# Performance work log

Measured on AMD Instinct MI355X. Metric: run time of the kernel, lower is better.

Reference implementation:

```python
import jax, jax.numpy as jnp
import numpy as np

DEPTH = 7  # complete binary trees with 2**DEPTH = 128 leaves

B, L = 4096, 128
V, E, OUT = 100000, 128, 3


def setup_inputs() -> dict:
    key = jax.random.key(0)
    ks = jax.random.split(key, 6)
    tokens = jax.random.randint(ks[0], (B, L), 0, V, dtype=jnp.int64)
    embedding = jax.random.normal(ks[1], (V, E), dtype=jnp.float32)
    # tree_layer: Linear(2E -> E); torch stores weight as [out, in]
    W_tree = jax.random.normal(ks[2], (E, 2 * E), dtype=jnp.float32) * (1.0 / np.sqrt(2 * E))
    b_tree = jax.random.normal(ks[3], (E,), dtype=jnp.float32) * 0.01
    # classifier_layer: Linear(E -> OUT)
    W_cls = jax.random.normal(ks[4], (OUT, E), dtype=jnp.float32) * (1.0 / np.sqrt(E))
    b_cls = jax.random.normal(ks[5], (OUT,), dtype=jnp.float32) * 0.01
    return {"tokens": tokens, "embedding": embedding, "W_tree": W_tree,
            "b_tree": b_tree, "W_cls": W_cls, "b_cls": b_cls}


def reference(tokens, embedding, W_tree, b_tree, W_cls, b_cls):
    # Leaf embeddings: gather rows of the embedding table. [B, L, E]
    reps = embedding[tokens]
    # Level-synchronous bottom-up composition (depth-batched across all trees):
    # at each level, pair adjacent nodes, concat features, apply tree_layer + tanh.
    for _ in range(DEPTH):
        left = reps[:, 0::2, :]   # [B, n/2, E]
        right = reps[:, 1::2, :]  # [B, n/2, E]
        combined = jnp.concatenate([left, right], axis=-1)  # [B, n/2, 2E]
        reps = jnp.tanh(jnp.einsum('bnh,eh->bne', combined, W_tree) + b_tree)
    roots = reps[:, 0, :]  # [B, E]
    return roots @ W_cls.T + b_cls  # [B, OUT]
```

## Files before the change

### kernel.cpp

```cpp
#include <hip/hip_runtime.h>
#include <hip/hip_fp16.h>


typedef _Float16 half8 __attribute__((ext_vector_type(8)));
typedef float floatx4 __attribute__((ext_vector_type(4)));

#define STRIDE 264
#define UROW   33
#define NPAIR  2048

__device__ __forceinline__ float fast_tanh(float x) {
  float e = __expf(2.f * x);
  return 1.f - 2.f * __builtin_amdgcn_rcpf(e + 1.f);
}

__device__ __forceinline__ unsigned pkrtz(float a, float b) {
  auto h = __builtin_amdgcn_cvt_pkrtz(a, b);
  return __builtin_bit_cast(unsigned, h);
}

__device__ __forceinline__ void gather_leafhalf(int tok, const float* __restrict__ emb,
                                                _Float16* buf, int row, int seg) {
  const float4* src = (const float4*)emb + (size_t)tok * 32 + (seg & 1) * 16;
  uint4* dst = (uint4*)buf + row * UROW + seg * 8;
#pragma unroll
  for (int j = 0; j < 8; ++j) {
    float4 x = src[2 * j], y = src[2 * j + 1];
    uint4 w;
    w.x = pkrtz(x.x, x.y); w.y = pkrtz(x.z, x.w);
    w.z = pkrtz(y.x, y.y); w.w = pkrtz(y.z, y.w);
    dst[j] = w;
  }
}

__device__ __forceinline__ void mfma_k256(const _Float16* arow, const half8 (&Wf)[2][8],
                                          floatx4 (&accO)[2]) {
  floatx4 aA[2], aB[2];
  aA[0] = (floatx4){0.f, 0.f, 0.f, 0.f}; aA[1] = (floatx4){0.f, 0.f, 0.f, 0.f};
  aB[0] = (floatx4){0.f, 0.f, 0.f, 0.f}; aB[1] = (floatx4){0.f, 0.f, 0.f, 0.f};
#pragma unroll
  for (int ks = 0; ks < 4; ++ks) {
    half8 x0 = *(const half8*)(arow + ks * 32);
    half8 x1 = *(const half8*)(arow + (ks + 4) * 32);
    aA[0] = __builtin_amdgcn_mfma_f32_16x16x32_f16(x0, Wf[0][ks],     aA[0], 0, 0, 0);
    aB[0] = __builtin_amdgcn_mfma_f32_16x16x32_f16(x1, Wf[0][ks + 4], aB[0], 0, 0, 0);
    aA[1] = __builtin_amdgcn_mfma_f32_16x16x32_f16(x0, Wf[1][ks],     aA[1], 0, 0, 0);
    aB[1] = __builtin_amdgcn_mfma_f32_16x16x32_f16(x1, Wf[1][ks + 4], aB[1], 0, 0, 0);
  }
  accO[0] = aA[0] + aB[0];
  accO[1] = aA[1] + aB[1];
}

template<int MT, int MOUT>
__device__ __forceinline__ void level_std(
    const _Float16* inb, _Float16* outb,
    const half8 (&Wf)[2][8], const float (&bias)[2],
    int nbase, int l15, int quad)
{
  floatx4 acc[MT][2];
  if (MT == 1) {
    floatx4 a2[2];
    mfma_k256(inb + l15 * STRIDE + quad * 8, Wf, a2);
    acc[0][0] = a2[0]; acc[0][1] = a2[1];
  } else {
#pragma unroll
    for (int m = 0; m < MT; ++m) {
      acc[m][0] = (floatx4){0.f, 0.f, 0.f, 0.f};
      acc[m][1] = (floatx4){0.f, 0.f, 0.f, 0.f};
    }
#pragma unroll
    for (int m = 0; m < MT; ++m) {
      const _Float16* arow = inb + (m * 16 + l15) * STRIDE + quad * 8;
#pragma unroll
      for (int ks = 0; ks < 8; ++ks) {
        half8 a = *(const half8*)(arow + ks * 32);
        acc[m][0] = __builtin_amdgcn_mfma_f32_16x16x32_f16(a, Wf[0][ks], acc[m][0], 0, 0, 0);
        acc[m][1] = __builtin_amdgcn_mfma_f32_16x16x32_f16(a, Wf[1][ks], acc[m][1], 0, 0, 0);
      }
    }
  }

  const int mrow = quad * 4;
#pragma unroll
  for (int m = 0; m < MT; ++m)
#pragma unroll
    for (int i = 0; i < 2; ++i) {
      const int col = (nbase + i) * 16 + l15;
#pragma unroll
      for (int r = 0; r < 4; ++r) {
        const int node = m * 16 + mrow + r;
        if (node < MOUT) {
          float v = fast_tanh(acc[m][i][r] + bias[i]);
          outb[(node >> 1) * STRIDE + (node & 1) * 128 + col] = (_Float16)v;
        }
      }
    }
}

__global__ __launch_bounds__(256, 3)
void tree_kernel(const int* __restrict__ tokens,
                 const float* __restrict__ embedding,
                 const float* __restrict__ W_tree,
                 const float* __restrict__ b_tree,
                 const float* __restrict__ W_cls,
                 const float* __restrict__ b_cls,
                 float* __restrict__ out)
{
  __shared__ __align__(16) _Float16 bufA[64 * STRIDE];
  __shared__ __align__(16) _Float16 bufB[32 * STRIDE];
  __shared__ __align__(16) _Float16 bufC[4 * STRIDE];
  __shared__ float wavepart[4][2][3];

  const int tid  = threadIdx.x;
  const int wid  = tid >> 6;
  const int lane = tid & 63;
  const int l15  = lane & 15;
  const int quad = lane >> 4;
  const int nbase = wid * 2;
  const int row  = tid & 63;
  const int seg  = tid >> 6;
  const int tidx = 2 * row + (seg >> 1);

  half8 Wf[2][8];
#pragma unroll
  for (int i = 0; i < 2; ++i) {
    const int e = (nbase + i) * 16 + l15;
#pragma unroll
    for (int ks = 0; ks < 8; ++ks) {
      const int k = ks * 32 + quad * 8;
      const float4* p = (const float4*)(W_tree + e * 256 + k);
      float4 lo = p[0], hi = p[1];
      half8 f;
      f[0] = (_Float16)lo.x; f[1] = (_Float16)lo.y; f[2] = (_Float16)lo.z; f[3] = (_Float16)lo.w;
      f[4] = (_Float16)hi.x; f[5] = (_Float16)hi.y; f[6] = (_Float16)hi.z; f[7] = (_Float16)hi.w;
      Wf[i][ks] = f;
    }
  }
  float bias[2];
#pragma unroll
  for (int i = 0; i < 2; ++i) bias[i] = b_tree[(nbase + i) * 16 + l15];

  float wc[2][3];
#pragma unroll
  for (int i = 0; i < 2; ++i) {
    const int col = (nbase + i) * 16 + l15;
#pragma unroll
    for (int o = 0; o < 3; ++o) wc[i][o] = W_cls[o * 128 + col];
  }

  int tokA = tokens[(2 * blockIdx.x) * 128 + tidx];

#pragma unroll 1
  for (int p = blockIdx.x; p < NPAIR; p += gridDim.x) {
    int pn = p + gridDim.x;
    if (pn >= NPAIR) pn = p;

    gather_leafhalf(tokA, embedding, bufA, row, seg);
    const int tokB = tokens[(2 * p + 1) * 128 + tidx];
    __syncthreads();

    level_std<4, 64>(bufA, bufB, Wf, bias, nbase, l15, quad);
    __syncthreads();
    level_std<2, 32>(bufB, bufA, Wf, bias, nbase, l15, quad);
    __syncthreads();
    level_std<1, 16>(bufA, bufB, Wf, bias, nbase, l15, quad);
    __syncthreads();
    level_std<1,  8>(bufB, bufA, Wf, bias, nbase, l15, quad);
    __syncthreads();
    level_std<1,  4>(bufA, bufC, Wf, bias, nbase, l15, quad);
    __syncthreads();

    gather_leafhalf(tokB, embedding, bufA, row, seg);
    tokA = tokens[(2 * pn) * 128 + tidx];
    __syncthreads();

    level_std<4, 64>(bufA, bufB, Wf, bias, nbase, l15, quad);
    __syncthreads();
    level_std<2, 32>(bufB, bufA, Wf, bias, nbase, l15, quad);
    __syncthreads();
    level_std<1, 16>(bufA, bufB, Wf, bias, nbase, l15, quad);
    __syncthreads();
    level_std<1,  8>(bufB, bufA, Wf, bias, nbase, l15, quad);
    __syncthreads();
    level_std<1,  4>(bufA, bufC + 2 * STRIDE, Wf, bias, nbase, l15, quad);
    __syncthreads();

    {
      const int rclamp = l15 < 4 ? l15 : 3;
      floatx4 acc[2];
      mfma_k256(bufC + rclamp * STRIDE + quad * 8, Wf, acc);
      const int mrow = quad * 4;
#pragma unroll
      for (int i = 0; i < 2; ++i) {
        const int col = (nbase + i) * 16 + l15;
#pragma unroll
        for (int r = 0; r < 4; ++r) {
          const int mr = mrow + r;
          if (mr < 4) {
            float v = fast_tanh(acc[i][r] + bias[i]);
            bufA[(mr >> 1) * STRIDE + (mr & 1) * 128 + col] = (_Float16)v;
          }
        }
      }
    }
    __syncthreads();

    {
      floatx4 acc[2];
      mfma_k256(bufA + l15 * STRIDE + quad * 8, Wf, acc);
      float part[2][3] = {{0.f, 0.f, 0.f}, {0.f, 0.f, 0.f}};
      if (quad == 0) {
#pragma unroll
        for (int i = 0; i < 2; ++i) {
#pragma unroll
          for (int rr = 0; rr < 2; ++rr) {
            float v = fast_tanh(acc[i][rr] + bias[i]);
#pragma unroll
            for (int o = 0; o < 3; ++o) part[rr][o] = fmaf(v, wc[i][o], part[rr][o]);
          }
        }
      }
#pragma unroll
      for (int rr = 0; rr < 2; ++rr) {
#pragma unroll
        for (int o = 0; o < 3; ++o) {
          float v = part[rr][o];
          v += __shfl_down(v, 8);
          v += __shfl_down(v, 4);
          v += __shfl_down(v, 2);
          v += __shfl_down(v, 1);
          if (lane == 0) wavepart[wid][rr][o] = v;
        }
      }
    }
    __syncthreads();
    if (tid < 6) {
      const int rr = tid / 3, o = tid - 3 * rr;
      float v = wavepart[0][rr][o] + wavepart[1][rr][o]
              + wavepart[2][rr][o] + wavepart[3][rr][o];
      out[(2 * p + rr) * 3 + o] = v + b_cls[o];
    }
  }
}

extern "C" void kernel_launch(void* const* d_in, const int* in_sizes, int n_in,
                              void* d_out, int out_size, void* d_ws, size_t ws_size,
                              hipStream_t stream) {
  const int*   tokens    = (const int*)d_in[0];
  const float* embedding = (const float*)d_in[1];
  const float* W_tree    = (const float*)d_in[2];
  const float* b_tree    = (const float*)d_in[3];
  const float* W_cls     = (const float*)d_in[4];
  const float* b_cls     = (const float*)d_in[5];
  float* out = (float*)d_out;

  dim3 grid(768), block(256);
  tree_kernel<<<grid, block, 0, stream>>>(tokens, embedding, W_tree, b_tree, W_cls, b_cls, out);
}
```

Before: 154.6 us.

## Prefetch next tree's embeddings into registers across levels and use lighter barriers

Splits the leaf gather into a global-load phase and a convert-and-store phase. Half of the next tree's embedding rows are issued into registers during the first level's compute, so gather latency overlaps with MFMA work. Replaces __syncthreads with a custom barrier that waits only on LDS counters, not global loads, so the in-flight prefetches do not stall the barrier. It also folds the bias into the accumulator init and splits the K loop into two chains for multi-tile levels. The trade-off is higher register pressure from holding 16 float4 prefetch registers, which may hurt occupancy at 3 blocks per CU.

```diff
diff --git a/kernel.cpp b/kernel.cpp
--- a/kernel.cpp
+++ b/kernel.cpp
@@ -9,6 +9,13 @@
 #define UROW   33
 #define NPAIR  2048
 
+__device__ __forceinline__ void bar() {
+  asm volatile("s_waitcnt lgkmcnt(0)" ::: "memory");
+  __builtin_amdgcn_sched_barrier(0);
+  __builtin_amdgcn_s_barrier();
+  __builtin_amdgcn_sched_barrier(0);
+}
+
 __device__ __forceinline__ float fast_tanh(float x) {
   float e = __expf(2.f * x);
   return 1.f - 2.f * __builtin_amdgcn_rcpf(e + 1.f);
@@ -19,25 +26,34 @@
   return __builtin_bit_cast(unsigned, h);
 }
 
-__device__ __forceinline__ void gather_leafhalf(int tok, const float* __restrict__ emb,
-                                                _Float16* buf, int row, int seg) {
-  const float4* src = (const float4*)emb + (size_t)tok * 32 + (seg & 1) * 16;
-  uint4* dst = (uint4*)buf + row * UROW + seg * 8;
-#pragma unroll
-  for (int j = 0; j < 8; ++j) {
-    float4 x = src[2 * j], y = src[2 * j + 1];
+__device__ __forceinline__ void load8(const float* __restrict__ emb, int tok, int seg,
+                                      int h, float4 (&x)[8]) {
+  const float4* src = (const float4*)emb + (size_t)tok * 32 + (seg & 1) * 16 + 8 * h;
+#pragma unroll
+  for (int j = 0; j < 8; ++j) x[j] = src[j];
+}
+
+__device__ __forceinline__ void gather_cvt_write(const float4 (&x)[8], _Float16* buf,
+                                                 int row, int seg, int h) {
+  uint4* dst = (uint4*)buf + row * UROW + seg * 8 + 4 * h;
+#pragma unroll
+  for (int j = 0; j < 4; ++j) {
+    float4 a = x[2 * j], b = x[2 * j + 1];
     uint4 w;
-    w.x = pkrtz(x.x, x.y); w.y = pkrtz(x.z, x.w);
-    w.z = pkrtz(y.x, y.y); w.w = pkrtz(y.z, y.w);
+    w.x = pkrtz(a.x, a.y); w.y = pkrtz(a.z, a.w);
+    w.z = pkrtz(b.x, b.y); w.w = pkrtz(b.z, b.w);
     dst[j] = w;
   }
 }
 
 __device__ __forceinline__ void mfma_k256(const _Float16* arow, const half8 (&Wf)[2][8],
-                                          floatx4 (&accO)[2]) {
+                                          const float (&bias)[2], floatx4 (&accO)[2]) {
   floatx4 aA[2], aB[2];
-  aA[0] = (floatx4){0.f, 0.f, 0.f, 0.f}; aA[1] = (floatx4){0.f, 0.f, 0.f, 0.f};
-  aB[0] = (floatx4){0.f, 0.f, 0.f, 0.f}; aB[1] = (floatx4){0.f, 0.f, 0.f, 0.f};
+#pragma unroll
+  for (int i = 0; i < 2; ++i) {
+    aA[i] = (floatx4){bias[i], bias[i], bias[i], bias[i]};
+    aB[i] = (floatx4){0.f, 0.f, 0.f, 0.f};
+  }
 #pragma unroll
   for (int ks = 0; ks < 4; ++ks) {
     half8 x0 = *(const half8*)(arow + ks * 32);
@@ -58,26 +74,11 @@
     int nbase, int l15, int quad)
 {
   floatx4 acc[MT][2];
-  if (MT == 1) {
+#pragma unroll
+  for (int m = 0; m < MT; ++m) {
     floatx4 a2[2];
-    mfma_k256(inb + l15 * STRIDE + quad * 8, Wf, a2);
-    acc[0][0] = a2[0]; acc[0][1] = a2[1];
-  } else {
-#pragma unroll
-    for (int m = 0; m < MT; ++m) {
-      acc[m][0] = (floatx4){0.f, 0.f, 0.f, 0.f};
-      acc[m][1] = (floatx4){0.f, 0.f, 0.f, 0.f};
-    }
-#pragma unroll
-    for (int m = 0; m < MT; ++m) {
-      const _Float16* arow = inb + (m * 16 + l15) * STRIDE + quad * 8;
-#pragma unroll
-      for (int ks = 0; ks < 8; ++ks) {
-        half8 a = *(const half8*)(arow + ks * 32);
-        acc[m][0] = __builtin_amdgcn_mfma_f32_16x16x32_f16(a, Wf[0][ks], acc[m][0], 0, 0, 0);
-        acc[m][1] = __builtin_amdgcn_mfma_f32_16x16x32_f16(a, Wf[1][ks], acc[m][1], 0, 0, 0);
-      }
-    }
+    mfma_k256(inb + (m * 16 + l15) * STRIDE + quad * 8, Wf, bias, a2);
+    acc[m][0] = a2[0]; acc[m][1] = a2[1];
   }
 
   const int mrow = quad * 4;
@@ -90,7 +91,7 @@
       for (int r = 0; r < 4; ++r) {
         const int node = m * 16 + mrow + r;
         if (node < MOUT) {
-          float v = fast_tanh(acc[m][i][r] + bias[i]);
+          float v = fast_tanh(acc[m][i][r]);
           outb[(node >> 1) * STRIDE + (node & 1) * 128 + col] = (_Float16)v;
         }
       }
@@ -149,46 +150,57 @@
   }
 
   int tokA = tokens[(2 * blockIdx.x) * 128 + tidx];
+  int tokB = tokens[(2 * blockIdx.x + 1) * 128 + tidx];
+  float4 pfA[8];
+  load8(embedding, tokA, seg, 0, pfA);
 
 #pragma unroll 1
   for (int p = blockIdx.x; p < NPAIR; p += gridDim.x) {
     int pn = p + gridDim.x;
     if (pn >= NPAIR) pn = p;
 
-    gather_leafhalf(tokA, embedding, bufA, row, seg);
-    const int tokB = tokens[(2 * p + 1) * 128 + tidx];
-    __syncthreads();
+    float4 x1[8];
+    load8(embedding, tokA, seg, 1, x1);
+    const int tokAn = tokens[(2 * pn) * 128 + tidx];
+    const int tokBn = tokens[(2 * pn + 1) * 128 + tidx];
+    gather_cvt_write(pfA, bufA, row, seg, 0);
+    gather_cvt_write(x1,  bufA, row, seg, 1);
+    bar();
 
     level_std<4, 64>(bufA, bufB, Wf, bias, nbase, l15, quad);
-    __syncthreads();
+    float4 pfB[8];
+    load8(embedding, tokB, seg, 0, pfB);
+    bar();
     level_std<2, 32>(bufB, bufA, Wf, bias, nbase, l15, quad);
-    __syncthreads();
+    bar();
     level_std<1, 16>(bufA, bufB, Wf, bias, nbase, l15, quad);
-    __syncthreads();
+    bar();
     level_std<1,  8>(bufB, bufA, Wf, bias, nbase, l15, quad);
-    __syncthreads();
+    bar();
     level_std<1,  4>(bufA, bufC, Wf, bias, nbase, l15, quad);
-    __syncthreads();
-
-    gather_leafhalf(tokB, embedding, bufA, row, seg);
-    tokA = tokens[(2 * pn) * 128 + tidx];
-    __syncthreads();
+    bar();
+
+    load8(embedding, tokB, seg, 1, x1);
+    gather_cvt_write(pfB, bufA, row, seg, 0);
+    gather_cvt_write(x1,  bufA, row, seg, 1);
+    bar();
 
     level_std<4, 64>(bufA, bufB, Wf, bias, nbase, l15, quad);
-    __syncthreads();
+    load8(embedding, tokAn, seg, 0, pfA);
+    bar();
     level_std<2, 32>(bufB, bufA, Wf, bias, nbase, l15, quad);
-    __syncthreads();
+    bar();
     level_std<1, 16>(bufA, bufB, Wf, bias, nbase, l15, quad);
-    __syncthreads();
+    bar();
     level_std<1,  8>(bufB, bufA, Wf, bias, nbase, l15, quad);
-    __syncthreads();
+    bar();
     level_std<1,  4>(bufA, bufC + 2 * STRIDE, Wf, bias, nbase, l15, quad);
-    __syncthreads();
+    bar();
 
     {
       const int rclamp = l15 < 4 ? l15 : 3;
       floatx4 acc[2];
-      mfma_k256(bufC + rclamp * STRIDE + quad * 8, Wf, acc);
+      mfma_k256(bufC + rclamp * STRIDE + quad * 8, Wf, bias, acc);
       const int mrow = quad * 4;
 #pragma unroll
       for (int i = 0; i < 2; ++i) {
@@ -197,24 +209,24 @@
         for (int r = 0; r < 4; ++r) {
           const int mr = mrow + r;
           if (mr < 4) {
-            float v = fast_tanh(acc[i][r] + bias[i]);
+            float v = fast_tanh(acc[i][r]);
             bufA[(mr >> 1) * STRIDE + (mr & 1) * 128 + col] = (_Float16)v;
           }
         }
       }
     }
-    __syncthreads();
+    bar();
 
     {
       floatx4 acc[2];
-      mfma_k256(bufA + l15 * STRIDE + quad * 8, Wf, acc);
+      mfma_k256(bufA + l15 * STRIDE + quad * 8, Wf, bias, acc);
       float part[2][3] = {{0.f, 0.f, 0.f}, {0.f, 0.f, 0.f}};
       if (quad == 0) {
 #pragma unroll
         for (int i = 0; i < 2; ++i) {
 #pragma unroll
           for (int rr = 0; rr < 2; ++rr) {
-            float v = fast_tanh(acc[i][rr] + bias[i]);
+            float v = fast_tanh(acc[i][rr]);
 #pragma unroll
             for (int o = 0; o < 3; ++o) part[rr][o] = fmaf(v, wc[i][o], part[rr][o]);
           }
@@ -233,13 +245,14 @@
         }
       }
     }
-    __syncthreads();
+    bar();
     if (tid < 6) {
       const int rr = tid / 3, o = tid - 3 * rr;
       float v = wavepart[0][rr][o] + wavepart[1][rr][o]
               + wavepart[2][rr][o] + wavepart[3][rr][o];
       out[(2 * p + rr) * 3 + o] = v + b_cls[o];
     }
+    tokA = tokAn; tokB = tokBn;
   }
 }
 
```

Result: no change. 157.6 us (+1.9%).

## Re-tile tree MFMA work as 2x2 wave grid with 64-column weight slices

Applied to the files above, without the earlier changes.

Waves are now split into two row groups and two column halves, each holding 64 output columns of W_tree in registers (double the weight registers) instead of 32. Each A-fragment loaded from LDS now feeds four MFMAs rather than two, which cuts LDS reads per MFMA. The bias is folded into the accumulator initialisation, and the next pair's tokens are prefetched one iteration ahead. In exchange, the small upper levels run on only two of four waves, leaving half the waves idle. Register pressure rises, which may hurt occupancy under launch_bounds(256,3).

```diff
diff --git a/kernel.cpp b/kernel.cpp
--- a/kernel.cpp
+++ b/kernel.cpp
@@ -33,68 +33,42 @@
   }
 }
 
-__device__ __forceinline__ void mfma_k256(const _Float16* arow, const half8 (&Wf)[2][8],
-                                          floatx4 (&accO)[2]) {
-  floatx4 aA[2], aB[2];
-  aA[0] = (floatx4){0.f, 0.f, 0.f, 0.f}; aA[1] = (floatx4){0.f, 0.f, 0.f, 0.f};
-  aB[0] = (floatx4){0.f, 0.f, 0.f, 0.f}; aB[1] = (floatx4){0.f, 0.f, 0.f, 0.f};
-#pragma unroll
-  for (int ks = 0; ks < 4; ++ks) {
-    half8 x0 = *(const half8*)(arow + ks * 32);
-    half8 x1 = *(const half8*)(arow + (ks + 4) * 32);
-    aA[0] = __builtin_amdgcn_mfma_f32_16x16x32_f16(x0, Wf[0][ks],     aA[0], 0, 0, 0);
-    aB[0] = __builtin_amdgcn_mfma_f32_16x16x32_f16(x1, Wf[0][ks + 4], aB[0], 0, 0, 0);
-    aA[1] = __builtin_amdgcn_mfma_f32_16x16x32_f16(x0, Wf[1][ks],     aA[1], 0, 0, 0);
-    aB[1] = __builtin_amdgcn_mfma_f32_16x16x32_f16(x1, Wf[1][ks + 4], aB[1], 0, 0, 0);
-  }
-  accO[0] = aA[0] + aB[0];
-  accO[1] = aA[1] + aB[1];
-}
-
-template<int MT, int MOUT>
-__device__ __forceinline__ void level_std(
-    const _Float16* inb, _Float16* outb,
-    const half8 (&Wf)[2][8], const float (&bias)[2],
-    int nbase, int l15, int quad)
+__device__ __forceinline__ void mfma_k256_n4(const _Float16* arow, const half8 (&Wf)[4][8],
+                                             const float (&bias)[4], floatx4 (&acc)[4]) {
+#pragma unroll
+  for (int i = 0; i < 4; ++i) acc[i] = (floatx4){bias[i], bias[i], bias[i], bias[i]};
+#pragma unroll
+  for (int ks = 0; ks < 8; ++ks) {
+    half8 x = *(const half8*)(arow + ks * 32);
+#pragma unroll
+    for (int i = 0; i < 4; ++i)
+      acc[i] = __builtin_amdgcn_mfma_f32_16x16x32_f16(x, Wf[i][ks], acc[i], 0, 0, 0);
+  }
+}
+
+template<int MT_LOC, int MOUT>
+__device__ __forceinline__ void level4(const _Float16* inb, _Float16* outb,
+                                       const half8 (&Wf)[4][8], const float (&bias)[4],
+                                       int mbase, int col0, int l15, int quad)
 {
-  floatx4 acc[MT][2];
-  if (MT == 1) {
-    floatx4 a2[2];
-    mfma_k256(inb + l15 * STRIDE + quad * 8, Wf, a2);
-    acc[0][0] = a2[0]; acc[0][1] = a2[1];
-  } else {
-#pragma unroll
-    for (int m = 0; m < MT; ++m) {
-      acc[m][0] = (floatx4){0.f, 0.f, 0.f, 0.f};
-      acc[m][1] = (floatx4){0.f, 0.f, 0.f, 0.f};
-    }
-#pragma unroll
-    for (int m = 0; m < MT; ++m) {
-      const _Float16* arow = inb + (m * 16 + l15) * STRIDE + quad * 8;
-#pragma unroll
-      for (int ks = 0; ks < 8; ++ks) {
-        half8 a = *(const half8*)(arow + ks * 32);
-        acc[m][0] = __builtin_amdgcn_mfma_f32_16x16x32_f16(a, Wf[0][ks], acc[m][0], 0, 0, 0);
-        acc[m][1] = __builtin_amdgcn_mfma_f32_16x16x32_f16(a, Wf[1][ks], acc[m][1], 0, 0, 0);
-      }
-    }
-  }
-
-  const int mrow = quad * 4;
-#pragma unroll
-  for (int m = 0; m < MT; ++m)
-#pragma unroll
-    for (int i = 0; i < 2; ++i) {
-      const int col = (nbase + i) * 16 + l15;
+#pragma unroll 1
+  for (int m = 0; m < MT_LOC; ++m) {
+    floatx4 acc[4];
+    mfma_k256_n4(inb + ((mbase + m) * 16 + l15) * STRIDE + quad * 8, Wf, bias, acc);
+    const int mrow = (mbase + m) * 16 + quad * 4;
+#pragma unroll
+    for (int i = 0; i < 4; ++i) {
+      const int col = col0 + i * 16 + l15;
 #pragma unroll
       for (int r = 0; r < 4; ++r) {
-        const int node = m * 16 + mrow + r;
-        if (node < MOUT) {
-          float v = fast_tanh(acc[m][i][r] + bias[i]);
+        const int node = mrow + r;
+        if (MOUT == 64 || node < MOUT) {
+          float v = fast_tanh(acc[i][r]);
           outb[(node >> 1) * STRIDE + (node & 1) * 128 + col] = (_Float16)v;
         }
       }
     }
+  }
 }
 
 __global__ __launch_bounds__(256, 3)
@@ -109,22 +83,24 @@
   __shared__ __align__(16) _Float16 bufA[64 * STRIDE];
   __shared__ __align__(16) _Float16 bufB[32 * STRIDE];
   __shared__ __align__(16) _Float16 bufC[4 * STRIDE];
-  __shared__ float wavepart[4][2][3];
+  __shared__ float wavepart[2][2][3];
 
   const int tid  = threadIdx.x;
   const int wid  = tid >> 6;
   const int lane = tid & 63;
   const int l15  = lane & 15;
   const int quad = lane >> 4;
-  const int nbase = wid * 2;
+  const int wn   = wid & 1;
+  const int wm   = wid >> 1;
+  const int col0 = wn * 64;
   const int row  = tid & 63;
   const int seg  = tid >> 6;
   const int tidx = 2 * row + (seg >> 1);
 
-  half8 Wf[2][8];
-#pragma unroll
-  for (int i = 0; i < 2; ++i) {
-    const int e = (nbase + i) * 16 + l15;
+  half8 Wf[4][8];
+#pragma unroll
+  for (int i = 0; i < 4; ++i) {
+    const int e = col0 + i * 16 + l15;
 #pragma unroll
     for (int ks = 0; ks < 8; ++ks) {
       const int k = ks * 32 + quad * 8;
@@ -136,19 +112,12 @@
       Wf[i][ks] = f;
     }
   }
-  float bias[2];
-#pragma unroll
-  for (int i = 0; i < 2; ++i) bias[i] = b_tree[(nbase + i) * 16 + l15];
-
-  float wc[2][3];
-#pragma unroll
-  for (int i = 0; i < 2; ++i) {
-    const int col = (nbase + i) * 16 + l15;
-#pragma unroll
-    for (int o = 0; o < 3; ++o) wc[i][o] = W_cls[o * 128 + col];
-  }
+  float bias[4];
+#pragma unroll
+  for (int i = 0; i < 4; ++i) bias[i] = b_tree[col0 + i * 16 + l15];
 
   int tokA = tokens[(2 * blockIdx.x) * 128 + tidx];
+  int tokB = tokens[(2 * blockIdx.x + 1) * 128 + tidx];
 
 #pragma unroll 1
   for (int p = blockIdx.x; p < NPAIR; p += gridDim.x) {
@@ -156,48 +125,48 @@
     if (pn >= NPAIR) pn = p;
 
     gather_leafhalf(tokA, embedding, bufA, row, seg);
-    const int tokB = tokens[(2 * p + 1) * 128 + tidx];
-    __syncthreads();
-
-    level_std<4, 64>(bufA, bufB, Wf, bias, nbase, l15, quad);
-    __syncthreads();
-    level_std<2, 32>(bufB, bufA, Wf, bias, nbase, l15, quad);
-    __syncthreads();
-    level_std<1, 16>(bufA, bufB, Wf, bias, nbase, l15, quad);
-    __syncthreads();
-    level_std<1,  8>(bufB, bufA, Wf, bias, nbase, l15, quad);
-    __syncthreads();
-    level_std<1,  4>(bufA, bufC, Wf, bias, nbase, l15, quad);
+    const int tokAn = tokens[(2 * pn) * 128 + tidx];
+    const int tokBn = tokens[(2 * pn + 1) * 128 + tidx];
+    __syncthreads();
+
+    level4<2, 64>(bufA, bufB, Wf, bias, wm * 2, col0, l15, quad);
+    __syncthreads();
+    level4<1, 32>(bufB, bufA, Wf, bias, wm,     col0, l15, quad);
+    __syncthreads();
+    if (wm == 0) level4<1, 16>(bufA, bufB, Wf, bias, 0, col0, l15, quad);
+    __syncthreads();
+    if (wm == 0) level4<1,  8>(bufB, bufA, Wf, bias, 0, col0, l15, quad);
+    __syncthreads();
+    if (wm == 0) level4<1,  4>(bufA, bufC, Wf, bias, 0, col0, l15, quad);
     __syncthreads();
 
     gather_leafhalf(tokB, embedding, bufA, row, seg);
-    tokA = tokens[(2 * pn) * 128 + tidx];
-    __syncthreads();
-
-    level_std<4, 64>(bufA, bufB, Wf, bias, nbase, l15, quad);
-    __syncthreads();
-    level_std<2, 32>(bufB, bufA, Wf, bias, nbase, l15, quad);
-    __syncthreads();
-    level_std<1, 16>(bufA, bufB, Wf, bias, nbase, l15, quad);
-    __syncthreads();
-    level_std<1,  8>(bufB, bufA, Wf, bias, nbase, l15, quad);
-    __syncthreads();
-    level_std<1,  4>(bufA, bufC + 2 * STRIDE, Wf, bias, nbase, l15, quad);
-    __syncthreads();
-
-    {
+    __syncthreads();
+
+    level4<2, 64>(bufA, bufB, Wf, bias, wm * 2, col0, l15, quad);
+    __syncthreads();
+    level4<1, 32>(bufB, bufA, Wf, bias, wm,     col0, l15, quad);
+    __syncthreads();
+    if (wm == 0) level4<1, 16>(bufA, bufB, Wf, bias, 0, col0, l15, quad);
+    __syncthreads();
+    if (wm == 0) level4<1,  8>(bufB, bufA, Wf, bias, 0, col0, l15, quad);
+    __syncthreads();
+    if (wm == 0) level4<1,  4>(bufA, bufC + 2 * STRIDE, Wf, bias, 0, col0, l15, quad);
+    __syncthreads();
+
+    if (wm == 0) {
       const int rclamp = l15 < 4 ? l15 : 3;
-      floatx4 acc[2];
-      mfma_k256(bufC + rclamp * STRIDE + quad * 8, Wf, acc);
+      floatx4 acc[4];
+      mfma_k256_n4(bufC + rclamp * STRIDE + quad * 8, Wf, bias, acc);
       const int mrow = quad * 4;
 #pragma unroll
-      for (int i = 0; i < 2; ++i) {
-        const int col = (nbase + i) * 16 + l15;
+      for (int i = 0; i < 4; ++i) {
+        const int col = col0 + i * 16 + l15;
 #pragma unroll
         for (int r = 0; r < 4; ++r) {
           const int mr = mrow + r;
           if (mr < 4) {
-            float v = fast_tanh(acc[i][r] + bias[i]);
+            float v = fast_tanh(acc[i][r]);
             bufA[(mr >> 1) * STRIDE + (mr & 1) * 128 + col] = (_Float16)v;
           }
         }
@@ -205,23 +174,28 @@
     }
     __syncthreads();
 
-    {
-      floatx4 acc[2];
-      mfma_k256(bufA + l15 * STRIDE + quad * 8, Wf, acc);
+    if (wm == 0) {
+      float wc[4][3];
+#pragma unroll
+      for (int i = 0; i < 4; ++i)
+#pragma unroll
+        for (int o = 0; o < 3; ++o) wc[i][o] = W_cls[o * 128 + col0 + i * 16 + l15];
+
+      floatx4 acc[4];
+      mfma_k256_n4(bufA + l15 * STRIDE + quad * 8, Wf, bias, acc);
       float part[2][3] = {{0.f, 0.f, 0.f}, {0.f, 0.f, 0.f}};
       if (quad == 0) {
 #pragma unroll
-        for (int i = 0; i < 2; ++i) {
+        for (int i = 0; i < 4; ++i)
 #pragma unroll
           for (int rr = 0; rr < 2; ++rr) {
-            float v = fast_tanh(acc[i][rr] + bias[i]);
+            float v = fast_tanh(acc[i][rr]);
 #pragma unroll
             for (int o = 0; o < 3; ++o) part[rr][o] = fmaf(v, wc[i][o], part[rr][o]);
           }
-        }
       }
 #pragma unroll
-      for (int rr = 0; rr < 2; ++rr) {
+      for (int rr = 0; rr < 2; ++rr)
 #pragma unroll
         for (int o = 0; o < 3; ++o) {
           float v = part[rr][o];
@@ -229,17 +203,15 @@
           v += __shfl_down(v, 4);
           v += __shfl_down(v, 2);
           v += __shfl_down(v, 1);
-          if (lane == 0) wavepart[wid][rr][o] = v;
+          if (lane == 0) wavepart[wn][rr][o] = v;
         }
-      }
     }
     __syncthreads();
     if (tid < 6) {
       const int rr = tid / 3, o = tid - 3 * rr;
-      float v = wavepart[0][rr][o] + wavepart[1][rr][o]
-              + wavepart[2][rr][o] + wavepart[3][rr][o];
-      out[(2 * p + rr) * 3 + o] = v + b_cls[o];
-    }
+      out[(2 * p + rr) * 3 + o] = wavepart[0][rr][o] + wavepart[1][rr][o] + b_cls[o];
+    }
+    tokA = tokAn; tokB = tokBn;
   }
 }
 
```

Measured after the change: 539.0 us. 249% more time.

## Split blocks into 8 waves across M and N for tree levels

Applied to the files above, without the earlier changes.

Doubles the block to 512 threads so the 8 waves split the work over both M (node rows) and N (output columns) in the two large levels, and each thread gathers a quarter embedding row instead of a half. Smaller levels run only on the first four waves. The bias is folded into the MFMA accumulator init, and token prefetch for the next pair is moved earlier. More waves per block give more latency hiding for the gather and the large GEMM levels. The cost is idle waves and the same barrier count at the small levels, plus tighter register limits from the launch bounds.

```diff
diff --git a/kernel.cpp b/kernel.cpp
--- a/kernel.cpp
+++ b/kernel.cpp
@@ -19,12 +19,12 @@
   return __builtin_bit_cast(unsigned, h);
 }
 
-__device__ __forceinline__ void gather_leafhalf(int tok, const float* __restrict__ emb,
-                                                _Float16* buf, int row, int seg) {
-  const float4* src = (const float4*)emb + (size_t)tok * 32 + (seg & 1) * 16;
-  uint4* dst = (uint4*)buf + row * UROW + seg * 8;
-#pragma unroll
-  for (int j = 0; j < 8; ++j) {
+__device__ __forceinline__ void gather_quarter(int tok, const float* __restrict__ emb,
+                                               _Float16* buf, int row, int seg) {
+  const float4* src = (const float4*)emb + (size_t)tok * 32 + (seg & 3) * 8;
+  uint4* dst = (uint4*)buf + row * UROW + (seg >> 2) * 16 + (seg & 3) * 4;
+#pragma unroll
+  for (int j = 0; j < 4; ++j) {
     float4 x = src[2 * j], y = src[2 * j + 1];
     uint4 w;
     w.x = pkrtz(x.x, x.y); w.y = pkrtz(x.z, x.w);
@@ -34,10 +34,13 @@
 }
 
 __device__ __forceinline__ void mfma_k256(const _Float16* arow, const half8 (&Wf)[2][8],
-                                          floatx4 (&accO)[2]) {
+                                          const float (&bias)[2], floatx4 (&accO)[2]) {
   floatx4 aA[2], aB[2];
-  aA[0] = (floatx4){0.f, 0.f, 0.f, 0.f}; aA[1] = (floatx4){0.f, 0.f, 0.f, 0.f};
-  aB[0] = (floatx4){0.f, 0.f, 0.f, 0.f}; aB[1] = (floatx4){0.f, 0.f, 0.f, 0.f};
+#pragma unroll
+  for (int i = 0; i < 2; ++i) {
+    aA[i] = (floatx4){bias[i], bias[i], bias[i], bias[i]};
+    aB[i] = (floatx4){0.f, 0.f, 0.f, 0.f};
+  }
 #pragma unroll
   for (int ks = 0; ks < 4; ++ks) {
     half8 x0 = *(const half8*)(arow + ks * 32);
@@ -51,53 +54,33 @@
   accO[1] = aA[1] + aB[1];
 }
 
-template<int MT, int MOUT>
-__device__ __forceinline__ void level_std(
+template<int MT_LOC, int MOUT>
+__device__ __forceinline__ void level_ms(
     const _Float16* inb, _Float16* outb,
     const half8 (&Wf)[2][8], const float (&bias)[2],
-    int nbase, int l15, int quad)
+    int mbase, int nbase, int l15, int quad)
 {
-  floatx4 acc[MT][2];
-  if (MT == 1) {
-    floatx4 a2[2];
-    mfma_k256(inb + l15 * STRIDE + quad * 8, Wf, a2);
-    acc[0][0] = a2[0]; acc[0][1] = a2[1];
-  } else {
-#pragma unroll
-    for (int m = 0; m < MT; ++m) {
-      acc[m][0] = (floatx4){0.f, 0.f, 0.f, 0.f};
-      acc[m][1] = (floatx4){0.f, 0.f, 0.f, 0.f};
-    }
-#pragma unroll
-    for (int m = 0; m < MT; ++m) {
-      const _Float16* arow = inb + (m * 16 + l15) * STRIDE + quad * 8;
-#pragma unroll
-      for (int ks = 0; ks < 8; ++ks) {
-        half8 a = *(const half8*)(arow + ks * 32);
-        acc[m][0] = __builtin_amdgcn_mfma_f32_16x16x32_f16(a, Wf[0][ks], acc[m][0], 0, 0, 0);
-        acc[m][1] = __builtin_amdgcn_mfma_f32_16x16x32_f16(a, Wf[1][ks], acc[m][1], 0, 0, 0);
-      }
-    }
-  }
-
-  const int mrow = quad * 4;
-#pragma unroll
-  for (int m = 0; m < MT; ++m)
+#pragma unroll
+  for (int m = 0; m < MT_LOC; ++m) {
+    floatx4 acc[2];
+    mfma_k256(inb + ((mbase + m) * 16 + l15) * STRIDE + quad * 8, Wf, bias, acc);
+    const int mrow = (mbase + m) * 16 + quad * 4;
 #pragma unroll
     for (int i = 0; i < 2; ++i) {
       const int col = (nbase + i) * 16 + l15;
 #pragma unroll
       for (int r = 0; r < 4; ++r) {
-        const int node = m * 16 + mrow + r;
-        if (node < MOUT) {
-          float v = fast_tanh(acc[m][i][r] + bias[i]);
+        const int node = mrow + r;
+        if (MOUT == 64 || node < MOUT) {
+          float v = fast_tanh(acc[i][r]);
           outb[(node >> 1) * STRIDE + (node & 1) * 128 + col] = (_Float16)v;
         }
       }
     }
-}
-
-__global__ __launch_bounds__(256, 3)
+  }
+}
+
+__global__ __launch_bounds__(512, 6)
 void tree_kernel(const int* __restrict__ tokens,
                  const float* __restrict__ embedding,
                  const float* __restrict__ W_tree,
@@ -116,10 +99,12 @@
   const int lane = tid & 63;
   const int l15  = lane & 15;
   const int quad = lane >> 4;
-  const int nbase = wid * 2;
+  const int wn   = wid & 3;
+  const int wm   = wid >> 2;
+  const int nbase = wn * 2;
   const int row  = tid & 63;
   const int seg  = tid >> 6;
-  const int tidx = 2 * row + (seg >> 1);
+  const int tidx = 2 * row + (seg >> 2);
 
   half8 Wf[2][8];
 #pragma unroll
@@ -140,55 +125,48 @@
 #pragma unroll
   for (int i = 0; i < 2; ++i) bias[i] = b_tree[(nbase + i) * 16 + l15];
 
-  float wc[2][3];
-#pragma unroll
-  for (int i = 0; i < 2; ++i) {
-    const int col = (nbase + i) * 16 + l15;
-#pragma unroll
-    for (int o = 0; o < 3; ++o) wc[i][o] = W_cls[o * 128 + col];
-  }
-
   int tokA = tokens[(2 * blockIdx.x) * 128 + tidx];
+  int tokB = tokens[(2 * blockIdx.x + 1) * 128 + tidx];
 
 #pragma unroll 1
   for (int p = blockIdx.x; p < NPAIR; p += gridDim.x) {
     int pn = p + gridDim.x;
     if (pn >= NPAIR) pn = p;
 
-    gather_leafhalf(tokA, embedding, bufA, row, seg);
-    const int tokB = tokens[(2 * p + 1) * 128 + tidx];
-    __syncthreads();
-
-    level_std<4, 64>(bufA, bufB, Wf, bias, nbase, l15, quad);
-    __syncthreads();
-    level_std<2, 32>(bufB, bufA, Wf, bias, nbase, l15, quad);
-    __syncthreads();
-    level_std<1, 16>(bufA, bufB, Wf, bias, nbase, l15, quad);
-    __syncthreads();
-    level_std<1,  8>(bufB, bufA, Wf, bias, nbase, l15, quad);
-    __syncthreads();
-    level_std<1,  4>(bufA, bufC, Wf, bias, nbase, l15, quad);
-    __syncthreads();
-
-    gather_leafhalf(tokB, embedding, bufA, row, seg);
-    tokA = tokens[(2 * pn) * 128 + tidx];
-    __syncthreads();
-
-    level_std<4, 64>(bufA, bufB, Wf, bias, nbase, l15, quad);
-    __syncthreads();
-    level_std<2, 32>(bufB, bufA, Wf, bias, nbase, l15, quad);
-    __syncthreads();
-    level_std<1, 16>(bufA, bufB, Wf, bias, nbase, l15, quad);
-    __syncthreads();
-    level_std<1,  8>(bufB, bufA, Wf, bias, nbase, l15, quad);
-    __syncthreads();
-    level_std<1,  4>(bufA, bufC + 2 * STRIDE, Wf, bias, nbase, l15, quad);
-    __syncthreads();
-
-    {
+    gather_quarter(tokA, embedding, bufA, row, seg);
+    const int tokAn = tokens[(2 * pn) * 128 + tidx];
+    const int tokBn = tokens[(2 * pn + 1) * 128 + tidx];
+    __syncthreads();
+
+    level_ms<2, 64>(bufA, bufB, Wf, bias, wm * 2, nbase, l15, quad);
+    __syncthreads();
+    level_ms<1, 32>(bufB, bufA, Wf, bias, wm,     nbase, l15, quad);
+    __syncthreads();
+    if (wm == 0) level_ms<1, 16>(bufA, bufB, Wf, bias, 0, nbase, l15, quad);
+    __syncthreads();
+    if (wm == 0) level_ms<1,  8>(bufB, bufA, Wf, bias, 0, nbase, l15, quad);
+    __syncthreads();
+    if (wm == 0) level_ms<1,  4>(bufA, bufC, Wf, bias, 0, nbase, l15, quad);
+    __syncthreads();
+
+    gather_quarter(tokB, embedding, bufA, row, seg);
+    __syncthreads();
+
+    level_ms<2, 64>(bufA, bufB, Wf, bias, wm * 2, nbase, l15, quad);
+    __syncthreads();
+    level_ms<1, 32>(bufB, bufA, Wf, bias, wm,     nbase, l15, quad);
+    __syncthreads();
+    if (wm == 0) level_ms<1, 16>(bufA, bufB, Wf, bias, 0, nbase, l15, quad);
+    __syncthreads();
+    if (wm == 0) level_ms<1,  8>(bufB, bufA, Wf, bias, 0, nbase, l15, quad);
+    __syncthreads();
+    if (wm == 0) level_ms<1,  4>(bufA, bufC + 2 * STRIDE, Wf, bias, 0, nbase, l15, quad);
+    __syncthreads();
+
+    if (wm == 0) {
       const int rclamp = l15 < 4 ? l15 : 3;
       floatx4 acc[2];
-      mfma_k256(bufC + rclamp * STRIDE + quad * 8, Wf, acc);
+      mfma_k256(bufC + rclamp * STRIDE + quad * 8, Wf, bias, acc);
       const int mrow = quad * 4;
 #pragma unroll
       for (int i = 0; i < 2; ++i) {
@@ -197,7 +175,7 @@
         for (int r = 0; r < 4; ++r) {
           const int mr = mrow + r;
           if (mr < 4) {
-            float v = fast_tanh(acc[i][r] + bias[i]);
+            float v = fast_tanh(acc[i][r]);
             bufA[(mr >> 1) * STRIDE + (mr & 1) * 128 + col] = (_Float16)v;
           }
         }
@@ -205,23 +183,28 @@
     }
     __syncthreads();
 
-    {
+    if (wm == 0) {
+      float wc[2][3];
+#pragma unroll
+      for (int i = 0; i < 2; ++i)
+#pragma unroll
+        for (int o = 0; o < 3; ++o) wc[i][o] = W_cls[o * 128 + (nbase + i) * 16 + l15];
+
       floatx4 acc[2];
-      mfma_k256(bufA + l15 * STRIDE + quad * 8, Wf, acc);
+      mfma_k256(bufA + l15 * STRIDE + quad * 8, Wf, bias, acc);
       float part[2][3] = {{0.f, 0.f, 0.f}, {0.f, 0.f, 0.f}};
       if (quad == 0) {
 #pragma unroll
-        for (int i = 0; i < 2; ++i) {
+        for (int i = 0; i < 2; ++i)
 #pragma unroll
           for (int rr = 0; rr < 2; ++rr) {
-            float v = fast_tanh(acc[i][rr] + bias[i]);
+            float v = fast_tanh(acc[i][rr]);
 #pragma unroll
             for (int o = 0; o < 3; ++o) part[rr][o] = fmaf(v, wc[i][o], part[rr][o]);
           }
-        }
       }
 #pragma unroll
-      for (int rr = 0; rr < 2; ++rr) {
+      for (int rr = 0; rr < 2; ++rr)
 #pragma unroll
         for (int o = 0; o < 3; ++o) {
           float v = part[rr][o];
@@ -229,9 +212,8 @@
           v += __shfl_down(v, 4);
           v += __shfl_down(v, 2);
           v += __shfl_down(v, 1);
-          if (lane == 0) wavepart[wid][rr][o] = v;
+          if (lane == 0) wavepart[wn][rr][o] = v;
         }
-      }
     }
     __syncthreads();
     if (tid < 6) {
@@ -240,6 +222,7 @@
               + wavepart[2][rr][o] + wavepart[3][rr][o];
       out[(2 * p + rr) * 3 + o] = v + b_cls[o];
     }
+    tokA = tokAn; tokB = tokBn;
   }
 }
 
@@ -254,6 +237,6 @@
   const float* b_cls     = (const float*)d_in[5];
   float* out = (float*)d_out;
 
-  dim3 grid(768), block(256);
+  dim3 grid(768), block(512);
   tree_kernel<<<grid, block, 0, stream>>>(tokens, embedding, W_tree, b_tree, W_cls, b_cls, out);
 }
```

Result: slower. 404.9 us (+161.9%).
